# Performance work log

Measured on AMD Instinct MI355X. Metric: run time of the kernel, lower is better.

The kernel has to match this reference:

```python
import jax, jax.numpy as jnp
import numpy as np

B, L, C, H, K, P = 64, 2048, 128, 128, 64, 336
NUM_BLOCKS = 4
EPS = 1e-5


def _revin_norm(x):
    mean = jnp.mean(x, axis=1, keepdims=True)
    std = jnp.sqrt(jnp.var(x, axis=1, keepdims=True) + EPS)
    return (x - mean) / std, mean, std


def _bn(x, gamma, beta, ch_axis):
    # training-mode BatchNorm1d: stats over all axes except ch_axis
    axes = tuple(i for i in range(x.ndim) if i != ch_axis)
    mean = jnp.mean(x, axis=axes, keepdims=True)
    var = jnp.var(x, axis=axes, keepdims=True)
    shp = [1] * x.ndim
    shp[ch_axis] = -1
    return (x - mean) / jnp.sqrt(var + EPS) * gamma.reshape(shp) + beta.reshape(shp)


def _mixer_block(x, bn_t_g, bn_t_b, lin_t_w, lin_t_b, bn_f_g, bn_f_b,
                 lin_f1_w, lin_f1_b, lin_f2_w, lin_f2_b):
    # timestep mixer: BN treats seq dim as channels, Linear over seq dim
    y = _bn(x, bn_t_g, bn_t_b, 1)                       # [B,L,C]
    y = jnp.swapaxes(y, 1, 2)                           # [B,C,L]
    y = jax.nn.gelu(y @ lin_t_w + lin_t_b, approximate=False)
    y = jnp.swapaxes(y, 1, 2)
    x = x + y
    # feature mixer: BN over channel dim, 2-layer MLP over features
    y = jnp.swapaxes(x, 1, 2)                           # [B,C,L]
    y = _bn(y, bn_f_g, bn_f_b, 1)
    y = jnp.swapaxes(y, 1, 2)                           # [B,L,C]
    y = jax.nn.gelu(y @ lin_f1_w + lin_f1_b, approximate=False)
    y = y @ lin_f2_w + lin_f2_b
    return x + y


def _forward(x, bern_u, cluster_embeds, wq_w, wq_b, wk_w, wk_b, wv_w, wv_b,
             cm_w1, cm_b1, cm_w2, cm_b2, tm_w1, tm_b1, tm_w2, tm_b2,
             bn_t_g, bn_t_b, lin_t_w, lin_t_b, bn_f_g, bn_f_b,
             lin_f1_w, lin_f1_b, lin_f2_w, lin_f2_b, out_w, out_b):
    xn, _, _ = _revin_norm(x)                           # [B,L,C]
    # channel MLP -> token embeddings h_i
    h = jax.nn.relu(xn @ cm_w1 + cm_b1) @ cm_w2 + cm_b2  # [B,L,H]
    # cosine-similarity soft routing to codebook
    hn = h / (jnp.linalg.norm(h, axis=-1, keepdims=True) + 1e-8)
    cn = cluster_embeds / (jnp.linalg.norm(cluster_embeds, axis=-1, keepdims=True) + 1e-8)
    p = jax.nn.softmax(jnp.einsum('blh,kh->blk', hn, cn), axis=-1)   # [B,L,K]
    M = (bern_u < p).astype(x.dtype)                    # bernoulli sample via external uniforms
    # exp-attention between cluster queries and token keys, masked by M
    Q = cluster_embeds @ wq_w + wq_b                    # [K,H]
    Km = h @ wk_w + wk_b                                # [B,L,H]
    V = h @ wv_w + wv_b                                 # [B,L,H]
    scores = jnp.einsum('kh,blh->bkl', Q, Km) / jnp.sqrt(jnp.asarray(H, x.dtype))
    aw = jax.nn.softmax(jnp.exp(scores) * jnp.swapaxes(M, 1, 2), axis=-1)  # [B,K,L]
    ao = jnp.einsum('bkl,blh->bkh', aw, V)              # [B,K,H]
    upd = ao * jnp.mean(p, axis=1)[:, :, None]          # prob-weighted cluster update
    new_cluster_embeds = jnp.mean(upd, axis=0)          # [K,H] (EMA-style copy target)
    # temporal module on channel embeddings
    h2 = jax.nn.relu(h @ tm_w1 + tm_b1) @ tm_w2 + tm_b2  # [B,L,H], H==C
    z, mean2, std2 = _revin_norm(h2)                    # second 'norm' overwrites stats
    for _ in range(NUM_BLOCKS):
        z = _mixer_block(z, bn_t_g, bn_t_b, lin_t_w, lin_t_b,
                         bn_f_g, bn_f_b, lin_f1_w, lin_f1_b, lin_f2_w, lin_f2_b)
    y = jnp.swapaxes(jnp.swapaxes(z, 1, 2) @ out_w + out_b, 1, 2)    # [B,P,C]
    y = y * std2 + mean2                                # denorm with second-call stats
    return y, new_cluster_embeds


def setup_inputs() -> dict:
    key = jax.random.key(0)
    ks = iter(jax.random.split(key, 40))

    def lin_w(fan_in, shape):
        return jax.random.uniform(next(ks), shape, jnp.float32, -1.0, 1.0) / np.sqrt(fan_in).astype(np.float32)

    return {
        'x': jax.random.normal(next(ks), (B, L, C), jnp.float32),
        'bern_u': jax.random.uniform(next(ks), (B, L, K), jnp.float32),
        'cluster_embeds': jax.random.normal(next(ks), (K, H), jnp.float32),
        'wq_w': lin_w(H, (H, H)), 'wq_b': lin_w(H, (H,)),
        'wk_w': lin_w(H, (H, H)), 'wk_b': lin_w(H, (H,)),
        'wv_w': lin_w(H, (H, H)), 'wv_b': lin_w(H, (H,)),
        'cm_w1': lin_w(C, (C, H)), 'cm_b1': lin_w(C, (H,)),
        'cm_w2': lin_w(H, (H, H)), 'cm_b2': lin_w(H, (H,)),
        'tm_w1': lin_w(H, (H, H)), 'tm_b1': lin_w(H, (H,)),
        'tm_w2': lin_w(H, (H, H)), 'tm_b2': lin_w(H, (H,)),
        'bn_t_g': jnp.ones((L,), jnp.float32), 'bn_t_b': jnp.zeros((L,), jnp.float32),
        'lin_t_w': lin_w(L, (L, L)), 'lin_t_b': lin_w(L, (L,)),
        'bn_f_g': jnp.ones((C,), jnp.float32), 'bn_f_b': jnp.zeros((C,), jnp.float32),
        'lin_f1_w': lin_w(C, (C, H)), 'lin_f1_b': lin_w(C, (H,)),
        'lin_f2_w': lin_w(H, (H, C)), 'lin_f2_b': lin_w(H, (C,)),
        'out_w': lin_w(L, (L, P)), 'out_b': lin_w(L, (P,)),
    }


def reference(x, bern_u, cluster_embeds, wq_w, wq_b, wk_w, wk_b, wv_w, wv_b,
              cm_w1, cm_b1, cm_w2, cm_b2, tm_w1, tm_b1, tm_w2, tm_b2,
              bn_t_g, bn_t_b, lin_t_w, lin_t_b, bn_f_g, bn_f_b,
              lin_f1_w, lin_f1_b, lin_f2_w, lin_f2_b, out_w, out_b):
    return _forward(x, bern_u, cluster_embeds, wq_w, wq_b, wk_w, wk_b, wv_w, wv_b,
                    cm_w1, cm_b1, cm_w2, cm_b2, tm_w1, tm_b1, tm_w2, tm_b2,
                    bn_t_g, bn_t_b, lin_t_w, lin_t_b, bn_f_g, bn_f_b,
                    lin_f1_w, lin_f1_b, lin_f2_w, lin_f2_b, out_w, out_b)
```

## Files before the change

kernel.cpp:

```cpp
#include <hip/hip_runtime.h>
#include <math.h>

#define BB 64
#define LL 2048
#define CC 128
#define HH 128
#define KK 64
#define PP 336
#define EPSf 1e-5f

typedef __attribute__((ext_vector_type(8))) short short8v;
typedef __attribute__((ext_vector_type(4))) float float4v;

__device__ inline ushort f2bf(float f) {
    union { float f; unsigned u; } v; v.f = f;
    unsigned r = (v.u + 0x7FFFu + ((v.u >> 16) & 1u)) >> 16;
    return (ushort)r;
}
__device__ inline float bf2f(ushort h) {
    union { unsigned u; float f; } v; v.u = ((unsigned)h) << 16;
    return v.f;
}

__device__ inline float fast_gelu(float v) {
    float x = 0.70710678118654752f * v;
    float ax = fabsf(x);
    float t = 1.f / fmaf(0.3275911f, ax, 1.f);
    float p = t * fmaf(t, fmaf(t, fmaf(t, fmaf(t, 1.061405429f, -1.453152027f),
                                       1.421413741f), -0.284496736f), 0.254829592f);
    float er = fmaf(-p, __expf(-ax * ax), 1.f);
    er = (x < 0.f) ? -er : er;
    return 0.5f * v * (1.f + er);
}

__device__ __forceinline__ void async16(const ushort* g, ushort* l) {
    __builtin_amdgcn_global_load_lds(
        (const __attribute__((address_space(1))) void*)g,
        (__attribute__((address_space(3))) void*)l, 16, 0, 0);
}

__global__ __launch_bounds__(256)
void colstats_part_kernel(const float* __restrict__ x, float* __restrict__ part) {
    int b = blockIdx.y, chunk = blockIdx.x;
    int t = threadIdx.x;
    int c4 = (t & 31) * 4, rg = t >> 5;
    const float* xb = x + ((size_t)b * LL + chunk * 256) * CC;
    float4 s = make_float4(0.f, 0.f, 0.f, 0.f);
    float4 q = make_float4(0.f, 0.f, 0.f, 0.f);
    for (int l = rg; l < 256; l += 8) {
        float4 v = *(const float4*)(xb + (size_t)l * CC + c4);
        s.x += v.x; s.y += v.y; s.z += v.z; s.w += v.w;
        q.x += v.x * v.x; q.y += v.y * v.y; q.z += v.z * v.z; q.w += v.w * v.w;
    }
    __shared__ float ls[8][128];
    __shared__ float lq[8][128];
    *(float4*)&ls[rg][c4] = s;
    *(float4*)&lq[rg][c4] = q;
    __syncthreads();
    if (t < 128) {
        float a = 0.f, d = 0.f;
        #pragma unroll
        for (int i = 0; i < 8; ++i) { a += ls[i][t]; d += lq[i][t]; }
        part[((size_t)b * 8 + chunk) * 256 + t] = a;
        part[((size_t)b * 8 + chunk) * 256 + 128 + t] = d;
    }
}

__global__ void colstats_final_kernel(const float* __restrict__ part, float* __restrict__ mean,
                                      float* __restrict__ rstd, float* __restrict__ stdv) {
    int b = blockIdx.x, c = threadIdx.x;
    float s = 0.f, q = 0.f;
    #pragma unroll
    for (int i = 0; i < 8; ++i) {
        s += part[((size_t)b * 8 + i) * 256 + c];
        q += part[((size_t)b * 8 + i) * 256 + 128 + c];
    }
    float mu = s * (1.f / LL);
    float var = q * (1.f / LL) - mu * mu;
    var = fmaxf(var, 0.f);
    float sd = sqrtf(var + EPSf);
    mean[b * CC + c] = mu;
    stdv[b * CC + c] = sd;
    rstd[b * CC + c] = 1.f / sd;
}

__global__ void colstats2_final_kernel(const float* __restrict__ cpart, float* __restrict__ mean,
                                       float* __restrict__ rstd, float* __restrict__ stdv) {
    int b = blockIdx.x, c = threadIdx.x;
    float s = 0.f, q = 0.f;
    #pragma unroll
    for (int i = 0; i < 16; ++i) {
        s += cpart[((size_t)b * 16 + i) * 256 + c];
        q += cpart[((size_t)b * 16 + i) * 256 + 128 + c];
    }
    float mu = s * (1.f / LL);
    float var = q * (1.f / LL) - mu * mu;
    var = fmaxf(var, 0.f);
    float sd = sqrtf(var + EPSf);
    mean[b * CC + c] = mu;
    stdv[b * CC + c] = sd;
    rstd[b * CC + c] = 1.f / sd;
}

__global__ void rn_final_kernel(const float* __restrict__ rsq, float* __restrict__ rn) {
    size_t i = (size_t)blockIdx.x * 256 + threadIdx.x;
    rn[i] = 1.f / (sqrtf(rsq[i]) + 1e-8f);
}

__global__ __launch_bounds__(256)
void gemm_kernel(const float* __restrict__ A, const float* __restrict__ W,
                 const float* __restrict__ bias, float* __restrict__ Out,
                 int M, int N, int Kd, int lda, int ldw, int ldo) {
    __shared__ float As[32][128];
    __shared__ float Ws[32][128];
    int tid = threadIdx.x;
    int tx = tid & 15, ty = tid >> 4;
    int n0 = blockIdx.x * 128;
    int m0 = blockIdx.y * 128;
    float acc[8][8] = {};

    for (int kt = 0; kt < Kd; kt += 32) {
        __syncthreads();
        #pragma unroll
        for (int it = 0; it < 4; ++it) {
            int q = tid + it * 256;
            int row = q >> 3;
            int kq = (q & 7) << 2;
            float4 v = make_float4(0.f, 0.f, 0.f, 0.f);
            int m = m0 + row;
            if (m < M) v = *(const float4*)(A + (size_t)m * lda + kt + kq);
            As[kq    ][row] = v.x;
            As[kq + 1][row] = v.y;
            As[kq + 2][row] = v.z;
            As[kq + 3][row] = v.w;
        }
        #pragma unroll
        for (int it = 0; it < 4; ++it) {
            int q = tid + it * 256;
            int kr = q >> 5;
            int nc = (q & 31) << 2;
            int n = n0 + nc;
            float4 v = make_float4(0.f, 0.f, 0.f, 0.f);
            if (n < N) v = *(const float4*)(W + (size_t)(kt + kr) * ldw + n);
            *(float4*)&Ws[kr][nc] = v;
        }
        __syncthreads();
        #pragma unroll
        for (int k = 0; k < 32; ++k) {
            float a[8], w[8];
            *(float4*)&a[0] = *(const float4*)&As[k][ty * 8];
            *(float4*)&a[4] = *(const float4*)&As[k][ty * 8 + 4];
            *(float4*)&w[0] = *(const float4*)&Ws[k][tx * 4];
            *(float4*)&w[4] = *(const float4*)&Ws[k][64 + tx * 4];
            #pragma unroll
            for (int i = 0; i < 8; ++i)
                #pragma unroll
                for (int j = 0; j < 8; ++j)
                    acc[i][j] = fmaf(a[i], w[j], acc[i][j]);
        }
    }

    #pragma unroll
    for (int i = 0; i < 8; ++i) {
        int m = m0 + ty * 8 + i;
        if (m >= M) continue;
        #pragma unroll
        for (int jj = 0; jj < 8; jj += 4) {
            int n = n0 + (jj ? 64 + tx * 4 : tx * 4);
            if (n >= N) continue;
            float o[4];
            #pragma unroll
            for (int j = 0; j < 4; ++j)
                o[j] = acc[i][jj + j] + (bias ? bias[n + j] : 0.f);
            *(float4*)(Out + (size_t)m * ldo + n) = *(float4*)o;
        }
    }
}

template <int NORM, int ACT, int EP>
__global__ __launch_bounds__(256)
void mfma_sq_kernel(const float* __restrict__ A, const ushort* __restrict__ Whi,
                    const ushort* __restrict__ Wlo, const float* __restrict__ bias,
                    float* Out,
                    const float* __restrict__ nmu, const float* __restrict__ ns,
                    const float* __restrict__ nt, int normStride,
                    ushort* __restrict__ hbOut) {
    __shared__ ushort Ahi[128][72];
    __shared__ ushort Alo[128][72];
    __shared__ ushort Bhi[128][72];
    __shared__ ushort Blo[128][72];
    int tid = threadIdx.x;
    int m0 = blockIdx.x * 128;
    int noff = (NORM == 1) ? (m0 / LL) * normStride : 0;

    int w = tid >> 6, lane = tid & 63;
    int wm = (w >> 1) * 64, wn = (w & 1) * 64;
    int col = lane & 15, kq = lane >> 4;

    float4v acc[4][4];
    #pragma unroll
    for (int i = 0; i < 4; ++i)
        #pragma unroll
        for (int j = 0; j < 4; ++j) acc[i][j] = (float4v){0.f, 0.f, 0.f, 0.f};

    for (int kt = 0; kt < 2; ++kt) {
        __syncthreads();
        #pragma unroll
        for (int it = 0; it < 4; ++it) {
            int q = tid + it * 256;
            int row = q >> 3, k0 = (q & 7) * 8;
            int kg = kt * 64 + k0;
            const float* ap = A + (size_t)(m0 + row) * 128 + kg;
            float vv[8];
            *(float4*)&vv[0] = *(const float4*)ap;
            *(float4*)&vv[4] = *(const float4*)(ap + 4);
            ushort hi[8], lo[8];
            #pragma unroll
            for (int j = 0; j < 8; ++j) {
                float v = vv[j];
                if (NORM == 1) v = (v - nmu[noff + kg + j]) * ns[noff + kg + j];
                if (NORM == 2) v = (v - nmu[kg + j]) * ns[kg + j] + nt[kg + j];
                ushort h = f2bf(v);
                hi[j] = h;
                lo[j] = f2bf(v - bf2f(h));
            }
            if (hbOut)
                *(short8v*)(hbOut + (size_t)(m0 + row) * 128 + kg) = *(short8v*)hi;
            *(short8v*)&Ahi[row][k0] = *(short8v*)hi;
            *(short8v*)&Alo[row][k0] = *(short8v*)lo;
        }
        #pragma unroll
        for (int it = 0; it < 4; ++it) {
            int q = tid + it * 256;
            int row = q >> 3, k0 = (q & 7) * 8;
            *(short8v*)&Bhi[row][k0] =
                *(const short8v*)(Whi + (size_t)row * 128 + kt * 64 + k0);
            *(short8v*)&Blo[row][k0] =
                *(const short8v*)(Wlo + (size_t)row * 128 + kt * 64 + k0);
        }
        __syncthreads();
        #pragma unroll
        for (int ksub = 0; ksub < 2; ++ksub) {
            short8v ah[4], al[4], bh[4], bl[4];
            #pragma unroll
            for (int mf = 0; mf < 4; ++mf) {
                ah[mf] = *(const short8v*)&Ahi[wm + mf * 16 + col][ksub * 32 + kq * 8];
                al[mf] = *(const short8v*)&Alo[wm + mf * 16 + col][ksub * 32 + kq * 8];
            }
            #pragma unroll
            for (int nf = 0; nf < 4; ++nf) {
                bh[nf] = *(const short8v*)&Bhi[wn + nf * 16 + col][ksub * 32 + kq * 8];
                bl[nf] = *(const short8v*)&Blo[wn + nf * 16 + col][ksub * 32 + kq * 8];
            }
            #pragma unroll
            for (int mf = 0; mf < 4; ++mf)
                #pragma unroll
                for (int nf = 0; nf < 4; ++nf)
                    acc[mf][nf] = __builtin_amdgcn_mfma_f32_16x16x32_bf16(
                        ah[mf], bh[nf], acc[mf][nf], 0, 0, 0);
            #pragma unroll
            for (int mf = 0; mf < 4; ++mf)
                #pragma unroll
                for (int nf = 0; nf < 4; ++nf)
                    acc[mf][nf] = __builtin_amdgcn_mfma_f32_16x16x32_bf16(
                        ah[mf], bl[nf], acc[mf][nf], 0, 0, 0);
            #pragma unroll
            for (int mf = 0; mf < 4; ++mf)
                #pragma unroll
                for (int nf = 0; nf < 4; ++nf)
                    acc[mf][nf] = __builtin_amdgcn_mfma_f32_16x16x32_bf16(
                        al[mf], bh[nf], acc[mf][nf], 0, 0, 0);
        }
    }

    int rbase = kq * 4;
    #pragma unroll
    for (int nf = 0; nf < 4; ++nf) {
        int n = wn + nf * 16 + col;
        if (EP == 2 && n >= 64) continue;
        float bn = bias ? bias[n] : 0.f;
        #pragma unroll
        for (int mf = 0; mf < 4; ++mf) {
            #pragma unroll
            for (int r = 0; r < 4; ++r) {
                int m = m0 + wm + mf * 16 + rbase + r;
                float v = acc[mf][nf][r] + bn;
                if (ACT == 1) v = fmaxf(v, 0.f);
                if (ACT == 2) v = fast_gelu(v);
                if (EP == 0) Out[(size_t)m * 128 + n] = v;
                else if (EP == 1) Out[(size_t)m * 128 + n] += v;
                else Out[(size_t)m * 64 + n] = v;
            }
        }
    }
}

template <int NORM, int ACT1, int ACT2, int EP2, int PREC>
__global__ __launch_bounds__(256)
void mfma_sq2_kernel(const float* __restrict__ A,
                     const ushort* __restrict__ W1h, const ushort* __restrict__ W1l,
                     const float* __restrict__ b1v,
                     const ushort* __restrict__ W2h, const ushort* __restrict__ W2l,
                     const float* __restrict__ b2v, float* Out,
                     const float* __restrict__ nmu, const float* __restrict__ ns,
                     const float* __restrict__ nt, int normStride,
                     float* __restrict__ rsum, float* __restrict__ rsq) {
    __shared__ ushort Xhi[128][72];
    __shared__ ushort Xlo[PREC ? 128 : 1][72];
    __shared__ ushort Bh[128][72];
    __shared__ ushort Bl[PREC ? 128 : 1][72];
    int tid = threadIdx.x;
    int m0 = blockIdx.x * 128;
    int noff = (NORM == 1) ? (m0 / LL) * normStride : 0;
    int w = tid >> 6, lane = tid & 63;
    int wm = (w >> 1) * 64, wn = (w & 1) * 64;
    int col = lane & 15, kq = lane >> 4;

    float4v acc[4][4];
    #pragma unroll
    for (int i = 0; i < 4; ++i)
        #pragma unroll
        for (int j = 0; j < 4; ++j) acc[i][j] = (float4v){0.f, 0.f, 0.f, 0.f};

    for (int kt = 0; kt < 2; ++kt) {
        __syncthreads();
        #pragma unroll
        for (int it = 0; it < 4; ++it) {
            int q = tid + it * 256;
            int row = q >> 3, k0 = (q & 7) * 8;
            int kg = kt * 64 + k0;
            const float* ap = A + (size_t)(m0 + row) * 128 + kg;
            float vv[8];
            *(float4*)&vv[0] = *(const float4*)ap;
            *(float4*)&vv[4] = *(const float4*)(ap + 4);
            ushort hi[8], lo[8];
            #pragma unroll
            for (int j = 0; j < 8; ++j) {
                float v = vv[j];
                if (NORM == 1) v = (v - nmu[noff + kg + j]) * ns[noff + kg + j];
                if (NORM == 2) v = (v - nmu[kg + j]) * ns[kg + j] + nt[kg + j];
                ushort h = f2bf(v);
                hi[j] = h;
                if (PREC) lo[j] = f2bf(v - bf2f(h));
            }
            *(short8v*)&Xhi[row][k0] = *(short8v*)hi;
            if (PREC) *(short8v*)&Xlo[row][k0] = *(short8v*)lo;
        }
        #pragma unroll
        for (int it = 0; it < 4; ++it) {
            int q = tid + it * 256;
            int row = q >> 3, k0 = (q & 7) * 8;
            *(short8v*)&Bh[row][k0] =
                *(const short8v*)(W1h + (size_t)row * 128 + kt * 64 + k0);
            if (PREC)
                *(short8v*)&Bl[row][k0] =
                    *(const short8v*)(W1l + (size_t)row * 128 + kt * 64 + k0);
        }
        __syncthreads();
        #pragma unroll
        for (int ksub = 0; ksub < 2; ++ksub) {
            short8v ah[4], al[4], bh[4], bl[4];
            #pragma unroll
            for (int mf = 0; mf < 4; ++mf) {
                ah[mf] = *(const short8v*)&Xhi[wm + mf * 16 + col][ksub * 32 + kq * 8];
                if (PREC) al[mf] = *(const short8v*)&Xlo[wm + mf * 16 + col][ksub * 32 + kq * 8];
            }
            #pragma unroll
            for (int nf = 0; nf < 4; ++nf) {
                bh[nf] = *(const short8v*)&Bh[wn + nf * 16 + col][ksub * 32 + kq * 8];
                if (PREC) bl[nf] = *(const short8v*)&Bl[wn + nf * 16 + col][ksub * 32 + kq * 8];
            }
            #pragma unroll
            for (int mf = 0; mf < 4; ++mf)
                #pragma unroll
                for (int nf = 0; nf < 4; ++nf)
                    acc[mf][nf] = __builtin_amdgcn_mfma_f32_16x16x32_bf16(
                        ah[mf], bh[nf], acc[mf][nf], 0, 0, 0);
            if (PREC) {
                #pragma unroll
                for (int mf = 0; mf < 4; ++mf)
                    #pragma unroll
                    for (int nf = 0; nf < 4; ++nf)
                        acc[mf][nf] = __builtin_amdgcn_mfma_f32_16x16x32_bf16(
                            ah[mf], bl[nf], acc[mf][nf], 0, 0, 0);
                #pragma unroll
                for (int mf = 0; mf < 4; ++mf)
                    #pragma unroll
                    for (int nf = 0; nf < 4; ++nf)
                        acc[mf][nf] = __builtin_amdgcn_mfma_f32_16x16x32_bf16(
                            al[mf], bh[nf], acc[mf][nf], 0, 0, 0);
            }
        }
    }

    float4v acc2[4][4];
    #pragma unroll
    for (int i = 0; i < 4; ++i)
        #pragma unroll
        for (int j = 0; j < 4; ++j) acc2[i][j] = (float4v){0.f, 0.f, 0.f, 0.f};

    for (int kt2 = 0; kt2 < 2; ++kt2) {
        __syncthreads();
        if ((wn >> 6) == kt2) {
            #pragma unroll
            for (int nf = 0; nf < 4; ++nf) {
                float bn = b1v[wn + nf * 16 + col];
                #pragma unroll
                for (int mf = 0; mf < 4; ++mf) {
                    #pragma unroll
                    for (int r = 0; r < 4; ++r) {
                        float v = acc[mf][nf][r] + bn;
                        if (ACT1 == 1) v = fmaxf(v, 0.f);
                        if (ACT1 == 2) v = fast_gelu(v);
                        int row = wm + mf * 16 + kq * 4 + r;
                        int c2 = nf * 16 + col;
                        ushort h = f2bf(v);
                        Xhi[row][c2] = h;
                        if (PREC) Xlo[row][c2] = f2bf(v - bf2f(h));
                    }
                }
            }
        }
        #pragma unroll
        for (int it = 0; it < 4; ++it) {
            int q = tid + it * 256;
            int row = q >> 3, k0 = (q & 7) * 8;
            *(short8v*)&Bh[row][k0] =
                *(const short8v*)(W2h + (size_t)row * 128 + kt2 * 64 + k0);
            if (PREC)
                *(short8v*)&Bl[row][k0] =
                    *(const short8v*)(W2l + (size_t)row * 128 + kt2 * 64 + k0);
        }
        __syncthreads();
        #pragma unroll
        for (int ksub = 0; ksub < 2; ++ksub) {
            short8v ah[4], al[4], bh[4], bl[4];
            #pragma unroll
            for (int mf = 0; mf < 4; ++mf) {
                ah[mf] = *(const short8v*)&Xhi[wm + mf * 16 + col][ksub * 32 + kq * 8];
                if (PREC) al[mf] = *(const short8v*)&Xlo[wm + mf * 16 + col][ksub * 32 + kq * 8];
            }
            #pragma unroll
            for (int nf = 0; nf < 4; ++nf) {
                bh[nf] = *(const short8v*)&Bh[wn + nf * 16 + col][ksub * 32 + kq * 8];
                if (PREC) bl[nf] = *(const short8v*)&Bl[wn + nf * 16 + col][ksub * 32 + kq * 8];
            }
            #pragma unroll
            for (int mf = 0; mf < 4; ++mf)
                #pragma unroll
                for (int nf = 0; nf < 4; ++nf)
                    acc2[mf][nf] = __builtin_amdgcn_mfma_f32_16x16x32_bf16(
                        ah[mf], bh[nf], acc2[mf][nf], 0, 0, 0);
            if (PREC) {
                #pragma unroll
                for (int mf = 0; mf < 4; ++mf)
                    #pragma unroll
                    for (int nf = 0; nf < 4; ++nf)
                        acc2[mf][nf] = __builtin_amdgcn_mfma_f32_16x16x32_bf16(
                            ah[mf], bl[nf], acc2[mf][nf], 0, 0, 0);
                #pragma unroll
                for (int mf = 0; mf < 4; ++mf)
                    #pragma unroll
                    for (int nf = 0; nf < 4; ++nf)
                        acc2[mf][nf] = __builtin_amdgcn_mfma_f32_16x16x32_bf16(
                            al[mf], bh[nf], acc2[mf][nf], 0, 0, 0);
            }
        }
    }

    int rbase = kq * 4;
    float rs_[4][4];
    float rq_[4][4];
    float cs_[4], cq_[4];
    if (EP2 == 1 || EP2 == 3) {
        #pragma unroll
        for (int a = 0; a < 4; ++a)
            #pragma unroll
            for (int b = 0; b < 4; ++b) { rs_[a][b] = 0.f; rq_[a][b] = 0.f; }
    }
    if (EP2 == 2) {
        #pragma unroll
        for (int a = 0; a < 4; ++a) { cs_[a] = 0.f; cq_[a] = 0.f; }
    }
    #pragma unroll
    for (int nf = 0; nf < 4; ++nf) {
        int n = wn + nf * 16 + col;
        float bn = b2v[n];
        #pragma unroll
        for (int mf = 0; mf < 4; ++mf) {
            #pragma unroll
            for (int r = 0; r < 4; ++r) {
                int m = m0 + wm + mf * 16 + rbase + r;
                float v = acc2[mf][nf][r] + bn;
                if (ACT2 == 1) v = fmaxf(v, 0.f);
                if (ACT2 == 2) v = fast_gelu(v);
                if (EP2 == 1) {
                    float fin = Out[(size_t)m * 128 + n] + v;
                    Out[(size_t)m * 128 + n] = fin;
                    rs_[mf][r] += fin;
                    rq_[mf][r] += fin * fin;
                } else {
                    Out[(size_t)m * 128 + n] = v;
                    if (EP2 == 2) { cs_[nf] += v; cq_[nf] += v * v; }
                    if (EP2 == 3) rq_[mf][r] += v * v;
                }
            }
        }
    }
    if (EP2 == 1) {
        #pragma unroll
        for (int mf = 0; mf < 4; ++mf)
            #pragma unroll
            for (int r = 0; r < 4; ++r) {
                float s = rs_[mf][r], q = rq_[mf][r];
                #pragma unroll
                for (int o = 1; o <= 8; o <<= 1) {
                    s += __shfl_xor(s, o);
                    q += __shfl_xor(q, o);
                }
                rs_[mf][r] = s; rq_[mf][r] = q;
            }
        __syncthreads();
        float* sred = (float*)&Xhi[0][0];
        float* qred = sred + 256;
        if (col == 0) {
            #pragma unroll
            for (int mf = 0; mf < 4; ++mf)
                #pragma unroll
                for (int r = 0; r < 4; ++r) {
                    int row = wm + mf * 16 + kq * 4 + r;
                    sred[row * 2 + (wn >> 6)] = rs_[mf][r];
                    qred[row * 2 + (wn >> 6)] = rq_[mf][r];
                }
        }
        __syncthreads();
        if (tid < 128) {
            rsum[(size_t)m0 + tid] = sred[tid * 2] + sred[tid * 2 + 1];
            rsq[(size_t)m0 + tid]  = qred[tid * 2] + qred[tid * 2 + 1];
        }
    }
    if (EP2 == 3) {
        #pragma unroll
        for (int mf = 0; mf < 4; ++mf)
            #pragma unroll
            for (int r = 0; r < 4; ++r) {
                float q = rq_[mf][r];
                #pragma unroll
                for (int o = 1; o <= 8; o <<= 1) q += __shfl_xor(q, o);
                rq_[mf][r] = q;
            }
        __syncthreads();
        float* qred = (float*)&Xhi[0][0];
        if (col == 0) {
            #pragma unroll
            for (int mf = 0; mf < 4; ++mf)
                #pragma unroll
                for (int r = 0; r < 4; ++r) {
                    int row = wm + mf * 16 + kq * 4 + r;
                    qred[row * 2 + (wn >> 6)] = rq_[mf][r];
                }
        }
        __syncthreads();
        if (tid < 128)
            rsq[(size_t)m0 + tid] = qred[tid * 2] + qred[tid * 2 + 1];
    }
    if (EP2 == 2) {
        #pragma unroll
        for (int nf = 0; nf < 4; ++nf) {
            #pragma unroll
            for (int o = 16; o <= 32; o <<= 1) {
                cs_[nf] += __shfl_xor(cs_[nf], o);
                cq_[nf] += __shfl_xor(cq_[nf], o);
            }
        }
        __syncthreads();
        float* colS = (float*)&Xhi[0][0];
        float* colQ = colS + 256;
        if (kq == 0) {
            #pragma unroll
            for (int nf = 0; nf < 4; ++nf) {
                int n = wn + nf * 16 + col;
                colS[(wm >> 6) * 128 + n] = cs_[nf];
                colQ[(wm >> 6) * 128 + n] = cq_[nf];
            }
        }
        __syncthreads();
        if (tid < 128) {
            rsum[(size_t)blockIdx.x * 256 + tid] = colS[tid] + colS[128 + tid];
            rsum[(size_t)blockIdx.x * 256 + 128 + tid] = colQ[tid] + colQ[128 + tid];
        }
    }
}

__global__ void wsplit_kernel(const float* __restrict__ W, ushort* __restrict__ Whi,
                              ushort* __restrict__ Wlo) {
    __shared__ float t[32][33];
    int k0 = blockIdx.x * 32, n0 = blockIdx.y * 32;
    int tx = threadIdx.x, ty = threadIdx.y;
    for (int i = ty; i < 32; i += 8)
        t[i][tx] = W[(size_t)(k0 + i) * 128 + n0 + tx];
    __syncthreads();
    for (int i = ty; i < 32; i += 8) {
        float v = t[tx][i];
        ushort h = f2bf(v);
        Whi[(size_t)(n0 + i) * 128 + k0 + tx] = h;
        Wlo[(size_t)(n0 + i) * 128 + k0 + tx] = f2bf(v - bf2f(h));
    }
}

template <int EPM>
__global__ __launch_bounds__(256)
void mfma_gemm_kernel(const ushort* __restrict__ A, const ushort* __restrict__ W,
                      const float* __restrict__ bias, float* Z,
                      int N, int Kd, int LDO, int nx, int nwg,
                      const float* __restrict__ epS, const float* __restrict__ epM,
                      float* __restrict__ bnfP) {
    __shared__ __align__(16) ushort smem[32768];
    float (*Ol)[132] = (float(*)[132])smem;

    int bid = blockIdx.x;
    int cpx = nwg >> 3;
    int swz = (bid & 7) * cpx + (bid >> 3);
    int n0 = (swz % nx) * 128;
    int m0 = (swz / nx) * 128;

    int tid = threadIdx.x;
    int w = tid >> 6, lane = tid & 63;
    int wm = (w >> 1) * 64, wn = (w & 1) * 64;
    int col = lane & 15, kq = lane >> 4;

    int srow = lane >> 3;
    int scol = ((lane & 7) ^ srow) << 3;
    int xr = (col & 7) << 4;

    float4v acc[4][4];
    #pragma unroll
    for (int i = 0; i < 4; ++i)
        #pragma unroll
        for (int j = 0; j < 4; ++j) acc[i][j] = (float4v){0.f, 0.f, 0.f, 0.f};

    int kTiles = Kd >> 6;

    #pragma unroll
    for (int it = 0; it < 4; ++it) {
        int rb = (w << 5) + (it << 3);
        async16(A + (size_t)(m0 + rb + srow) * Kd + scol, smem + (rb << 6));
    }
    #pragma unroll
    for (int it = 0; it < 4; ++it) {
        int rb = (w << 5) + (it << 3);
        async16(W + (size_t)(n0 + rb + srow) * Kd + scol, smem + 8192 + (rb << 6));
    }
    __syncthreads();

    for (int kt = 0; kt < kTiles; ++kt) {
        int cur = kt & 1;
        ushort* Ac = smem + (cur << 14);
        ushort* Bc = Ac + 8192;
        if (kt + 1 < kTiles) {
            ushort* An = smem + ((cur ^ 1) << 14);
            ushort* Bn = An + 8192;
            int kb = (kt + 1) << 6;
            #pragma unroll
            for (int it = 0; it < 4; ++it) {
                int rb = (w << 5) + (it << 3);
                async16(A + (size_t)(m0 + rb + srow) * Kd + kb + scol, An + (rb << 6));
            }
            #pragma unroll
            for (int it = 0; it < 4; ++it) {
                int rb = (w << 5) + (it << 3);
                async16(W + (size_t)(n0 + rb + srow) * Kd + kb + scol, Bn + (rb << 6));
            }
        }
        __builtin_amdgcn_s_setprio(1);
        #pragma unroll
        for (int ksub = 0; ksub < 2; ++ksub) {
            int cswz = (((ksub << 6) + (kq << 4)) ^ xr) >> 1;
            short8v af[4], bf[4];
            #pragma unroll
            for (int mf = 0; mf < 4; ++mf)
                af[mf] = *(const short8v*)(Ac + (wm + mf * 16 + col) * 64 + cswz);
            #pragma unroll
            for (int nf = 0; nf < 4; ++nf)
                bf[nf] = *(const short8v*)(Bc + (wn + nf * 16 + col) * 64 + cswz);
            #pragma unroll
            for (int mf = 0; mf < 4; ++mf)
                #pragma unroll
                for (int nf = 0; nf < 4; ++nf)
                    acc[mf][nf] = __builtin_amdgcn_mfma_f32_16x16x32_bf16(
                        af[mf], bf[nf], acc[mf][nf], 0, 0, 0);
        }
        __builtin_amdgcn_s_setprio(0);
        __syncthreads();
    }

    int b = m0 >> 7;
    float cs[16], cq[16];
    if (EPM == 1) {
        #pragma unroll
        for (int k2 = 0; k2 < 16; ++k2) { cs[k2] = 0.f; cq[k2] = 0.f; }
    }
    #pragma unroll
    for (int q = 0; q < 4; ++q) {
        __syncthreads();
        #pragma unroll
        for (int nf = 0; nf < 4; ++nf) {
            int gnl = wn + nf * 16;
            if ((gnl >> 5) != q) continue;
            int gn = n0 + gnl + col;
            float bn = (EPM == 2 && gn >= N) ? 0.f : bias[gn];
            int nl = gnl - q * 32 + col;
            #pragma unroll
            for (int mf = 0; mf < 4; ++mf) {
                #pragma unroll
                for (int r = 0; r < 4; ++r) {
                    float v = acc[mf][nf][r] + bn;
                    if (EPM == 1) v = fast_gelu(v);
                    Ol[nl][wm + mf * 16 + kq * 4 + r] = v;
                }
            }
        }
        __syncthreads();
        int nloc = tid >> 3, c0 = (tid & 7) * 16;
        int gn = n0 + q * 32 + nloc;
        if ((EPM == 2 || EPM == 3) && gn >= N) continue;
        float* zr;
        if (EPM == 3)
            zr = Z + (((size_t)(m0 >> 11) * 64 + gn) * 2048) + (m0 & 2047) + c0;
        else
            zr = Z + ((size_t)b * LDO + gn) * CC + c0;
        #pragma unroll
        for (int i = 0; i < 4; ++i) {
            float4 v = *(float4*)&Ol[nloc][c0 + i * 4];
            if (EPM == 1) {
                float4 o = *(float4*)(zr + i * 4);
                v.x += o.x; v.y += o.y; v.z += o.z; v.w += o.w;
                *(float4*)(zr + i * 4) = v;
                cs[i * 4 + 0] += v.x; cs[i * 4 + 1] += v.y;
                cs[i * 4 + 2] += v.z; cs[i * 4 + 3] += v.w;
                cq[i * 4 + 0] += v.x * v.x; cq[i * 4 + 1] += v.y * v.y;
                cq[i * 4 + 2] += v.z * v.z; cq[i * 4 + 3] += v.w * v.w;
            } else if (EPM == 2) {
                int mb = m0 + c0 + i * 4;
                float4 s4 = *(const float4*)(epS + mb);
                float4 m4 = *(const float4*)(epM + mb);
                v.x = v.x * s4.x + m4.x; v.y = v.y * s4.y + m4.y;
                v.z = v.z * s4.z + m4.z; v.w = v.w * s4.w + m4.w;
                *(float4*)(zr + i * 4) = v;
            } else {
                *(float4*)(zr + i * 4) = v;
            }
        }
    }
    if (EPM == 1) {
        __syncthreads();
        float* sred = (float*)smem;
        float* qred = sred + 4096;
        int rrow = tid >> 3, cb = (tid & 7) * 16;
        #pragma unroll
        for (int k2 = 0; k2 < 16; ++k2) {
            sred[rrow * 128 + cb + k2] = cs[k2];
            qred[rrow * 128 + cb + k2] = cq[k2];
        }
        __syncthreads();
        if (tid < 128) {
            float a = 0.f;
            for (int r = 0; r < 32; ++r) a += sred[r * 128 + tid];
            bnfP[(size_t)bid * 256 + tid] = a;
        } else {
            int c = tid - 128;
            float a = 0.f;
            for (int r = 0; r < 32; ++r) a += qred[r * 128 + c];
            bnfP[(size_t)bid * 256 + 128 + c] = a;
        }
    }
}

__global__ void wtrans_kernel(const float* __restrict__ W, ushort* __restrict__ WT,
                              int Kd, int N) {
    __shared__ float t[32][33];
    int k0 = blockIdx.x * 32, n0 = blockIdx.y * 32;
    int tx = threadIdx.x, ty = threadIdx.y;
    for (int i = ty; i < 32; i += 8) {
        int n = n0 + tx;
        t[i][tx] = (n < N) ? W[(size_t)(k0 + i) * N + n] : 0.f;
    }
    __syncthreads();
    for (int i = ty; i < 32; i += 8)
        WT[(size_t)(n0 + i) * Kd + k0 + tx] = f2bf(t[tx][i]);
}

__global__ void cn_split_kernel(const float* __restrict__ ce, ushort* __restrict__ ch,
                                ushort* __restrict__ cl) {
    int k = blockIdx.x, h = threadIdx.x;
    if (k >= KK) {
        ch[(size_t)k * 128 + h] = 0;
        cl[(size_t)k * 128 + h] = 0;
        return;
    }
    __shared__ float sh[128];
    float v = ce[(size_t)k * HH + h];
    sh[h] = v * v;
    __syncthreads();
    for (int o = 64; o >= 1; o >>= 1) {
        if (h < o) sh[h] += sh[h + o];
        __syncthreads();
    }
    float nv = v / (sqrtf(sh[0]) + 1e-8f);
    ushort hh = f2bf(nv);
    ch[(size_t)k * 128 + h] = hh;
    cl[(size_t)k * 128 + h] = f2bf(nv - bf2f(hh));
}

__global__ void qprime_kernel(const float* __restrict__ Q, const float* __restrict__ wk_w,
                              const float* __restrict__ wk_b, ushort* __restrict__ qpb,
                              float* __restrict__ qbp) {
    int k = blockIdx.x;
    int hp = threadIdx.x;
    if (k >= KK) {
        qpb[(size_t)k * HH + hp] = 0;
        if (hp == 0) qbp[k] = 0.f;
        return;
    }
    __shared__ float qrow[128];
    __shared__ float red[128];
    qrow[hp] = Q[(size_t)k * HH + hp];
    __syncthreads();
    float s = 0.f;
    for (int h = 0; h < HH; ++h) s = fmaf(qrow[h], wk_w[(size_t)hp * HH + h], s);
    const float rs = 0.088388347648318447f;
    qpb[(size_t)k * HH + hp] = f2bf(s * rs);
    red[hp] = qrow[hp] * wk_b[hp];
    __syncthreads();
    for (int o = 64; o >= 1; o >>= 1) {
        if (hp < o) red[hp] += red[hp + o];
        __syncthreads();
    }
    if (hp == 0) qbp[k] = red[0] * rs;
}

__global__ __launch_bounds__(256)
void pmask_kernel(const float* __restrict__ sp, const float* __restrict__ rn,
                  const float* __restrict__ bern, unsigned char* __restrict__ Mt,
                  float* __restrict__ ppart) {
    int b = blockIdx.y;
    int l0 = blockIdx.x * 32;
    int tid = threadIdx.x;
    int wv = tid >> 6, lane = tid & 63;
    __shared__ float Msh[64][33];
    __shared__ float psum[4][64];
    float pa = 0.f;
    for (int tt = 0; tt < 8; ++tt) {
        int l = l0 + wv * 8 + tt;
        size_t tok = (size_t)b * LL + l;
        float s = sp[tok * 64 + lane] * rn[tok];
        float mx = s;
        #pragma unroll
        for (int o = 32; o >= 1; o >>= 1) mx = fmaxf(mx, __shfl_xor(mx, o));
        float ev = expf(s - mx);
        float sm = ev;
        #pragma unroll
        for (int o = 32; o >= 1; o >>= 1) sm += __shfl_xor(sm, o);
        float p = ev / sm;
        pa += p;
        Msh[lane][wv * 8 + tt] = (bern[tok * KK + lane] < p) ? 1.f : 0.f;
    }
    psum[wv][lane] = pa;
    __syncthreads();
    for (int q = tid; q < 64 * 32; q += 256) {
        int k = q >> 5, j = q & 31;
        Mt[((size_t)b * KK + k) * LL + l0 + j] = (unsigned char)Msh[k][j];
    }
    if (tid < 64)
        ppart[((size_t)b * (LL / 32) + blockIdx.x) * KK + tid] =
            psum[0][tid] + psum[1][tid] + psum[2][tid] + psum[3][tid];
}

__global__ void pmean_final_kernel(const float* __restrict__ part, float* __restrict__ pm) {
    int b = blockIdx.x, k = threadIdx.x;
    float s = 0.f;
    for (int i = 0; i < LL / 32; ++i) s += part[((size_t)b * (LL / 32) + i) * KK + k];
    pm[b * KK + k] = s * (1.f / LL);
}

__global__ __launch_bounds__(256)
void aw_kernel(float* __restrict__ S, const unsigned char* __restrict__ Mt) {
    size_t base = (size_t)blockIdx.x * LL;
    int tid = threadIdx.x;
    float t[8];
    float mx = -1e30f;
    #pragma unroll
    for (int i = 0; i < 8; ++i) {
        int l = tid + i * 256;
        float v = expf(S[base + l]) * (float)Mt[base + l];
        t[i] = v;
        mx = fmaxf(mx, v);
    }
    __shared__ float shA[4];
    __shared__ float shB[4];
    #pragma unroll
    for (int o = 32; o >= 1; o >>= 1) mx = fmaxf(mx, __shfl_xor(mx, o));
    if ((tid & 63) == 0) shA[tid >> 6] = mx;
    __syncthreads();
    mx = fmaxf(fmaxf(shA[0], shA[1]), fmaxf(shA[2], shA[3]));
    float e[8];
    float sum = 0.f;
    #pragma unroll
    for (int i = 0; i < 8; ++i) { e[i] = expf(t[i] - mx); sum += e[i]; }
    #pragma unroll
    for (int o = 32; o >= 1; o >>= 1) sum += __shfl_xor(sum, o);
    if ((tid & 63) == 0) shB[tid >> 6] = sum;
    __syncthreads();
    sum = (shB[0] + shB[1]) + (shB[2] + shB[3]);
    float inv = 1.f / sum;
    #pragma unroll
    for (int i = 0; i < 8; ++i) S[base + tid + i * 256] = e[i] * inv;
}

__global__ __launch_bounds__(256)
void awh_part_kernel(const float* __restrict__ AWs, const float* __restrict__ hmat,
                     float* __restrict__ part) {
    __shared__ float AT[32][64];
    __shared__ float VT[32][128];
    int b = blockIdx.y, sp = blockIdx.x;
    int tid = threadIdx.x;
    int tx = tid & 15, ty = tid >> 4;
    float acc[4][8] = {};
    const float* Ab = AWs + (size_t)b * KK * LL + sp * 512;
    const float* Vb = hmat + ((size_t)b * LL + sp * 512) * HH;
    for (int lt = 0; lt < 512; lt += 32) {
        __syncthreads();
        #pragma unroll
        for (int it = 0; it < 2; ++it) {
            int q = tid + it * 256;
            int row = q >> 3;
            int lq = (q & 7) << 2;
            float4 v = *(const float4*)(Ab + (size_t)row * LL + lt + lq);
            AT[lq][row] = v.x; AT[lq + 1][row] = v.y;
            AT[lq + 2][row] = v.z; AT[lq + 3][row] = v.w;
        }
        #pragma unroll
        for (int it = 0; it < 4; ++it) {
            int q = tid + it * 256;
            int lr = q >> 5;
            int hc = (q & 31) << 2;
            *(float4*)&VT[lr][hc] = *(const float4*)(Vb + (size_t)(lt + lr) * HH + hc);
        }
        __syncthreads();
        #pragma unroll
        for (int l = 0; l < 32; ++l) {
            float av[4], vv[8];
            *(float4*)&av[0] = *(const float4*)&AT[l][ty * 4];
            *(float4*)&vv[0] = *(const float4*)&VT[l][tx * 4];
            *(float4*)&vv[4] = *(const float4*)&VT[l][64 + tx * 4];
            #pragma unroll
            for (int i = 0; i < 4; ++i)
                #pragma unroll
                for (int j = 0; j < 8; ++j)
                    acc[i][j] = fmaf(av[i], vv[j], acc[i][j]);
        }
    }
    #pragma unroll
    for (int i = 0; i < 4; ++i) {
        int k = ty * 4 + i;
        #pragma unroll
        for (int jj = 0; jj < 8; jj += 4) {
            int h = (jj ? 64 + tx * 4 : tx * 4);
            float o[4];
            #pragma unroll
            for (int j = 0; j < 4; ++j) o[j] = acc[i][jj + j];
            *(float4*)(part + (((size_t)b * 4 + sp) * KK + k) * HH + h) = *(float4*)o;
        }
    }
}

__global__ void awh_reduce_kernel(const float* __restrict__ part, float* __restrict__ awh) {
    int bk = blockIdx.x, h = threadIdx.x;
    int b = bk >> 6, k = bk & 63;
    float s = 0.f;
    #pragma unroll
    for (int sp = 0; sp < 4; ++sp)
        s += part[(((size_t)b * 4 + sp) * KK + k) * HH + h];
    awh[(size_t)bk * HH + h] = s;
}

__global__ void newce_kernel(const float* __restrict__ ao, const float* __restrict__ pm,
                             float* __restrict__ outTail) {
    int k = blockIdx.x, h = threadIdx.x;
    float s = 0.f;
    for (int b = 0; b < BB; ++b)
        s += ao[((size_t)b * KK + k) * HH + h] * pm[b * KK + k];
    outTail[(size_t)k * HH + h] = s * (1.f / BB);
}

__global__ void revin_apply_kernel(const float* __restrict__ in, float* __restrict__ out,
                                   const float* __restrict__ mu, const float* __restrict__ rs,
                                   float* __restrict__ rsum, float* __restrict__ rsq) {
    int b = blockIdx.y;
    size_t base = (size_t)b * LL * CC + (size_t)blockIdx.x * 8192;
    int c0 = (threadIdx.x * 4) & 127;
    int lane = threadIdx.x & 63;
    float4 m4 = *(const float4*)(mu + b * CC + c0);
    float4 r4 = *(const float4*)(rs + b * CC + c0);
    #pragma unroll
    for (int j = 0; j < 8; ++j) {
        float4 v = *(const float4*)(in + base + threadIdx.x * 4 + j * 1024);
        v.x = (v.x - m4.x) * r4.x; v.y = (v.y - m4.y) * r4.y;
        v.z = (v.z - m4.z) * r4.z; v.w = (v.w - m4.w) * r4.w;
        *(float4*)(out + base + threadIdx.x * 4 + j * 1024) = v;
        float s = v.x + v.y + v.z + v.w;
        float q = v.x * v.x + v.y * v.y + v.z * v.z + v.w * v.w;
        #pragma unroll
        for (int o = 1; o <= 16; o <<= 1) {
            s += __shfl_xor(s, o);
            q += __shfl_xor(q, o);
        }
        if ((lane & 31) == 0) {
            size_t row = (base + (size_t)threadIdx.x * 4 + (size_t)j * 1024) >> 7;
            rsum[row] = s;
            rsq[row] = q;
        }
    }
}

__global__ void bnt_final_kernel(const float* __restrict__ rsum, const float* __restrict__ rsq,
                                 float* __restrict__ mu, float* __restrict__ rv) {
    int l = blockIdx.x * 256 + threadIdx.x;
    float s = 0.f, q = 0.f;
    for (int b = 0; b < BB; ++b) {
        s += rsum[(size_t)b * LL + l];
        q += rsq[(size_t)b * LL + l];
    }
    float m = s * (1.f / (BB * CC));
    float var = q * (1.f / (BB * CC)) - m * m;
    var = fmaxf(var, 0.f);
    mu[l] = m;
    rv[l] = 1.f / sqrtf(var + EPSf);
}

template <bool DO_BN>
__global__ __launch_bounds__(256)
void transpose_bn_kernel(const float* __restrict__ in, ushort* __restrict__ out,
                         const float* __restrict__ mu, const float* __restrict__ rv,
                         const float* __restrict__ g, const float* __restrict__ be) {
    __shared__ ushort tile[32][72];
    int l0 = blockIdx.x * 64, c0 = blockIdx.y * 32, b = blockIdx.z;
    int t = threadIdx.x;
    const float* ib = in + ((size_t)b * LL + l0) * CC + c0;
    #pragma unroll
    for (int it = 0; it < 2; ++it) {
        int idx = t + it * 256;
        int row = idx >> 3;
        int c = (idx & 7) * 4;
        float4 v = *(const float4*)(ib + (size_t)row * CC + c);
        if (DO_BN) {
            int l = l0 + row;
            float sc = rv[l] * g[l];
            float m = mu[l], bb = be[l];
            v.x = (v.x - m) * sc + bb; v.y = (v.y - m) * sc + bb;
            v.z = (v.z - m) * sc + bb; v.w = (v.w - m) * sc + bb;
        }
        tile[c    ][row] = f2bf(v.x);
        tile[c + 1][row] = f2bf(v.y);
        tile[c + 2][row] = f2bf(v.z);
        tile[c + 3][row] = f2bf(v.w);
    }
    __syncthreads();
    int cc = t >> 3, l8 = (t & 7) * 8;
    ushort* ob = out + (size_t)b * CC * LL + (size_t)(c0 + cc) * LL + l0 + l8;
    *(uint4*)ob = *(const uint4*)&tile[cc][l8];
}

__global__ void bnf_mid_kernel(const float* __restrict__ part, float* __restrict__ mid) {
    int gblk = blockIdx.x, t = threadIdx.x;
    float s = 0.f;
    #pragma unroll
    for (int i = 0; i < 16; ++i)
        s += part[(size_t)(gblk * 16 + i) * 256 + t];
    mid[(size_t)gblk * 256 + t] = s;
}

__global__ void bnf_final_kernel(const float* __restrict__ mid, const float* __restrict__ g,
                                 const float* __restrict__ be, float* __restrict__ mu,
                                 float* __restrict__ sA, float* __restrict__ tA) {
    int c = threadIdx.x;
    float s = 0.f, s2 = 0.f;
    #pragma unroll
    for (int i = 0; i < 64; ++i) {
        s += mid[(size_t)i * 256 + c];
        s2 += mid[(size_t)i * 256 + 128 + c];
    }
    float m = s / (float)(BB * LL);
    float var = s2 / (float)(BB * LL) - m * m;
    var = fmaxf(var, 0.f);
    float rvv = 1.f / sqrtf(var + EPSf);
    mu[c] = m;
    sA[c] = rvv * g[c];
    tA[c] = be[c];
}

extern "C" void kernel_launch(void* const* d_in, const int* in_sizes, int n_in,
                              void* d_out, int out_size, void* d_ws, size_t ws_size,
                              hipStream_t stream) {
    const float* x     = (const float*)d_in[0];
    const float* bern  = (const float*)d_in[1];
    const float* ce    = (const float*)d_in[2];
    const float* wq_w  = (const float*)d_in[3];
    const float* wq_b  = (const float*)d_in[4];
    const float* wk_w  = (const float*)d_in[5];
    const float* wk_b  = (const float*)d_in[6];
    const float* wv_w  = (const float*)d_in[7];
    const float* wv_b  = (const float*)d_in[8];
    const float* cm_w1 = (const float*)d_in[9];
    const float* cm_b1 = (const float*)d_in[10];
    const float* cm_w2 = (const float*)d_in[11];
    const float* cm_b2 = (const float*)d_in[12];
    const float* tm_w1 = (const float*)d_in[13];
    const float* tm_b1 = (const float*)d_in[14];
    const float* tm_w2 = (const float*)d_in[15];
    const float* tm_b2 = (const float*)d_in[16];
    const float* bn_t_g = (const float*)d_in[17];
    const float* bn_t_b = (const float*)d_in[18];
    const float* lin_t_w = (const float*)d_in[19];
    const float* lin_t_b = (const float*)d_in[20];
    const float* bn_f_g = (const float*)d_in[21];
    const float* bn_f_b = (const float*)d_in[22];
    const float* f1_w  = (const float*)d_in[23];
    const float* f1_b  = (const float*)d_in[24];
    const float* f2_w  = (const float*)d_in[25];
    const float* f2_b  = (const float*)d_in[26];
    const float* out_w = (const float*)d_in[27];
    const float* out_b = (const float*)d_in[28];
    (void)in_sizes; (void)n_in; (void)out_size;

    float* y = (float*)d_out;
    float* ceOut = y + (size_t)BB * PP * CC;

    float* ws = (float*)d_ws;
    size_t off = 0;
    auto alloc = [&](size_t n) { float* p = ws + off; off += n; return p; };
    float* mean1  = alloc(BB * CC);
    float* rstd1  = alloc(BB * CC);
    float* std1   = alloc(BB * CC);
    float* mean2  = alloc(BB * CC);
    float* rstd2  = alloc(BB * CC);
    float* std2   = alloc(BB * CC);
    float* bnmu   = alloc(LL);
    float* bnrv   = alloc(LL);
    float* bfpart = alloc(1024 * 256);
    float* bfmid  = alloc(64 * 256);
    float* bfmu   = alloc(CC);
    float* bfs    = alloc(CC);
    float* bft    = alloc(CC);
    float* cxpart = alloc(BB * 8 * 256);
    float* cpart2 = alloc(1024 * 256);
    float* qbuf   = alloc(KK * HH);
    ushort* qpb   = (ushort*)alloc(128 * 128 / 2);
    float* qbp    = alloc(128);
    ushort* cnbh  = (ushort*)alloc(8192);
    ushort* cnbl  = (ushort*)alloc(8192);
    float* rn     = alloc((size_t)BB * LL);
    float* rsum   = alloc((size_t)BB * LL);
    float* rsq    = alloc((size_t)BB * LL);
    float* ppart  = alloc((size_t)BB * (LL / 32) * KK);
    float* pmean  = alloc(BB * KK);
    float* awhprt = alloc((size_t)BB * 4 * KK * HH);
    float* awh    = alloc((size_t)BB * KK * HH);
    float* aobuf  = alloc((size_t)BB * KK * HH);
    ushort* wsp   = (ushort*)alloc(7 * 2 * 16384 / 2);
    ushort* wtT   = (ushort*)alloc((size_t)LL * LL / 2);
    ushort* owT   = (ushort*)alloc((size_t)384 * LL / 2);
    float* S      = alloc((size_t)BB * KK * LL);
    float* buf0   = alloc((size_t)BB * LL * CC);
    float* buf2   = alloc((size_t)BB * LL * CC);
    unsigned char* Mt = (unsigned char*)(ws + off);
    ushort* abf = (ushort*)S;
    ushort* hb  = (ushort*)buf0;
    (void)ws_size;

    auto whi = [&](int i) { return wsp + (size_t)i * 2 * 16384; };
    auto wlo = [&](int i) { return wsp + (size_t)i * 2 * 16384 + 16384; };

    const int ML = BB * LL;
    dim3 tb(32, 8);
    dim3 tgrid(LL / 64, CC / 32, BB);
    dim3 wsg(4, 4);

    wtrans_kernel<<<dim3(LL / 32, LL / 32), tb, 0, stream>>>(lin_t_w, wtT, LL, LL);
    wtrans_kernel<<<dim3(LL / 32, 12), tb, 0, stream>>>(out_w, owT, LL, PP);
    wsplit_kernel<<<wsg, tb, 0, stream>>>(cm_w1, whi(0), wlo(0));
    wsplit_kernel<<<wsg, tb, 0, stream>>>(cm_w2, whi(1), wlo(1));
    wsplit_kernel<<<wsg, tb, 0, stream>>>(tm_w1, whi(2), wlo(2));
    wsplit_kernel<<<wsg, tb, 0, stream>>>(tm_w2, whi(3), wlo(3));
    wsplit_kernel<<<wsg, tb, 0, stream>>>(f1_w, whi(4), wlo(4));
    wsplit_kernel<<<wsg, tb, 0, stream>>>(f2_w, whi(5), wlo(5));
    wsplit_kernel<<<wsg, tb, 0, stream>>>(wv_w, whi(6), wlo(6));

    colstats_part_kernel<<<dim3(8, BB), 256, 0, stream>>>(x, cxpart);
    colstats_final_kernel<<<dim3(BB), dim3(128), 0, stream>>>(cxpart, mean1, rstd1, std1);
    mfma_sq2_kernel<1, 1, 0, 3, 1><<<dim3(ML / 128), 256, 0, stream>>>(
        x, whi(0), wlo(0), cm_b1, whi(1), wlo(1), cm_b2, buf2, mean1, rstd1, nullptr, CC,
        nullptr, rsq);
    rn_final_kernel<<<dim3(ML / 256), 256, 0, stream>>>(rsq, rn);
    gemm_kernel<<<dim3(1, 1), 256, 0, stream>>>(ce, wq_w, wq_b, qbuf,
        KK, HH, HH, HH, HH, HH);
    qprime_kernel<<<dim3(128), dim3(128), 0, stream>>>(qbuf, wk_w, wk_b, qpb, qbp);
    cn_split_kernel<<<dim3(128), dim3(128), 0, stream>>>(ce, cnbh, cnbl);
    mfma_sq_kernel<0, 0, 2><<<dim3(ML / 128), 256, 0, stream>>>(
        buf2, cnbh, cnbl, nullptr, S, nullptr, nullptr, nullptr, 0, hb);
    pmask_kernel<<<dim3(LL / 32, BB), 256, 0, stream>>>(S, rn, bern, Mt, ppart);
    pmean_final_kernel<<<dim3(BB), dim3(64), 0, stream>>>(ppart, pmean);
    mfma_gemm_kernel<3><<<dim3(1024), 256, 0, stream>>>(
        hb, qpb, qbp, S, KK, 128, 0, 1, 1024, nullptr, nullptr, nullptr);
    aw_kernel<<<dim3(BB * KK), 256, 0, stream>>>(S, Mt);
    awh_part_kernel<<<dim3(4, BB), 256, 0, stream>>>(S, buf2, awhprt);
    awh_reduce_kernel<<<dim3(BB * KK), dim3(128), 0, stream>>>(awhprt, awh);
    mfma_sq_kernel<0, 0, 0><<<dim3((BB * KK) / 128), 256, 0, stream>>>(
        awh, whi(6), wlo(6), wv_b, aobuf, nullptr, nullptr, nullptr, 0, nullptr);
    newce_kernel<<<dim3(KK), dim3(128), 0, stream>>>(aobuf, pmean, ceOut);
    mfma_sq2_kernel<0, 1, 0, 2, 1><<<dim3(ML / 128), 256, 0, stream>>>(
        buf2, whi(2), wlo(2), tm_b1, whi(3), wlo(3), tm_b2, buf0,
        nullptr, nullptr, nullptr, 0, cpart2, nullptr);
    colstats2_final_kernel<<<dim3(BB), dim3(128), 0, stream>>>(cpart2, mean2, rstd2, std2);
    revin_apply_kernel<<<dim3(32, BB), 256, 0, stream>>>(buf0, buf2, mean2, rstd2, rsum, rsq);
    for (int blkI = 0; blkI < 4; ++blkI) {
        bnt_final_kernel<<<dim3(8), 256, 0, stream>>>(rsum, rsq, bnmu, bnrv);
        transpose_bn_kernel<true><<<tgrid, 256, 0, stream>>>(buf2, abf, bnmu, bnrv, bn_t_g, bn_t_b);
        mfma_gemm_kernel<1><<<dim3(1024), 256, 0, stream>>>(
            abf, wtT, lin_t_b, buf2, LL, LL, LL, 16, 1024, nullptr, nullptr, bfpart);
        bnf_mid_kernel<<<dim3(64), 256, 0, stream>>>(bfpart, bfmid);
        bnf_final_kernel<<<dim3(1), dim3(128), 0, stream>>>(bfmid, bn_f_g, bn_f_b, bfmu, bfs, bft);
        mfma_sq2_kernel<2, 2, 0, 1, 0><<<dim3(ML / 128), 256, 0, stream>>>(
            buf2, whi(4), wlo(4), f1_b, whi(5), wlo(5), f2_b, buf2, bfmu, bfs, bft, 0,
            rsum, rsq);
    }
    transpose_bn_kernel<false><<<tgrid, 256, 0, stream>>>(buf2, abf,
        nullptr, nullptr, nullptr, nullptr);
    mfma_gemm_kernel<2><<<dim3(192), 256, 0, stream>>>(
        abf, owT, out_b, y, PP, LL, PP, 3, 192, std2, mean2, nullptr);
}
```

Baseline: 1.261 ms.

## Add 512-thread triple-buffered MFMA kernel for timestep-mixer GEMM

Adds a dedicated kernel for the 2048x2048 timestep-mixer GEMM. It uses 512 threads (8 waves), triple-buffered async LDS staging with swizzled layout, explicit vmcnt waits and raised wave priority during the MFMA phase. The fused epilogue applies bias, GELU, the residual add and BN-f partial sums. The aim is better latency hiding and occupancy for the dominant GEMM inside the 4-block loop, at the cost of 96KB of dynamic shared memory per block and a fallback path.

```diff
diff --git a/kernel.cpp b/kernel.cpp
--- a/kernel.cpp
+++ b/kernel.cpp
@@ -605,6 +605,145 @@
         ushort h = f2bf(v);
         Whi[(size_t)(n0 + i) * 128 + k0 + tx] = h;
         Wlo[(size_t)(n0 + i) * 128 + k0 + tx] = f2bf(v - bf2f(h));
+    }
+}
+
+__global__ __launch_bounds__(512)
+void mfma_ts_kernel(const ushort* __restrict__ A, const ushort* __restrict__ W,
+                    const float* __restrict__ bias, float* Z,
+                    int nx, int nwg, float* __restrict__ bnfP) {
+    extern __shared__ __align__(16) ushort smem[];
+    float (*Ol)[132] = (float(*)[132])smem;
+
+    int bid = blockIdx.x;
+    int cpx = nwg >> 3;
+    int swz = (bid & 7) * cpx + (bid >> 3);
+    int n0 = (swz % nx) * 128;
+    int m0 = (swz / nx) * 128;
+
+    int tid = threadIdx.x;
+    int w = tid >> 6, lane = tid & 63;
+    int wm = (w >> 1) * 32, wn = (w & 1) * 64;
+    int col = lane & 15, kq = lane >> 4;
+    int srow = lane >> 3;
+    int scol = ((lane & 7) ^ srow) << 3;
+    int xr = (col & 7) << 4;
+
+    float4v acc[2][4];
+    #pragma unroll
+    for (int i = 0; i < 2; ++i)
+        #pragma unroll
+        for (int j = 0; j < 4; ++j) acc[i][j] = (float4v){0.f, 0.f, 0.f, 0.f};
+
+    const int kTiles = LL >> 6;
+
+    auto stage = [&](int kt2, int bsel) {
+        ushort* Ab = smem + bsel * 16384;
+        ushort* Bb = Ab + 8192;
+        int kb = kt2 << 6;
+        #pragma unroll
+        for (int it = 0; it < 2; ++it) {
+            int rb = w * 16 + it * 8;
+            async16(A + (size_t)(m0 + rb + srow) * LL + kb + scol, Ab + (rb << 6));
+            async16(W + (size_t)(n0 + rb + srow) * LL + kb + scol, Bb + (rb << 6));
+        }
+    };
+
+    stage(0, 0);
+    stage(1, 1);
+    int cur = 0;
+    for (int kt = 0; kt < kTiles; ++kt) {
+        if (kt + 1 < kTiles)
+            asm volatile("s_waitcnt vmcnt(4)" ::: "memory");
+        else
+            asm volatile("s_waitcnt vmcnt(0)" ::: "memory");
+        __builtin_amdgcn_s_barrier();
+        __builtin_amdgcn_sched_barrier(0);
+        if (kt + 2 < kTiles) {
+            int nb = cur + 2; if (nb >= 3) nb -= 3;
+            stage(kt + 2, nb);
+        }
+        const ushort* Ac = smem + cur * 16384;
+        const ushort* Bc = Ac + 8192;
+        __builtin_amdgcn_s_setprio(1);
+        #pragma unroll
+        for (int ksub = 0; ksub < 2; ++ksub) {
+            int cswz = (((ksub << 6) + (kq << 4)) ^ xr) >> 1;
+            short8v af[2], bf[4];
+            af[0] = *(const short8v*)(Ac + (wm + col) * 64 + cswz);
+            af[1] = *(const short8v*)(Ac + (wm + 16 + col) * 64 + cswz);
+            #pragma unroll
+            for (int nf = 0; nf < 4; ++nf)
+                bf[nf] = *(const short8v*)(Bc + (wn + nf * 16 + col) * 64 + cswz);
+            #pragma unroll
+            for (int mf = 0; mf < 2; ++mf)
+                #pragma unroll
+                for (int nf = 0; nf < 4; ++nf)
+                    acc[mf][nf] = __builtin_amdgcn_mfma_f32_16x16x32_bf16(
+                        af[mf], bf[nf], acc[mf][nf], 0, 0, 0);
+        }
+        __builtin_amdgcn_s_setprio(0);
+        ++cur; if (cur == 3) cur = 0;
+    }
+
+    int b = m0 >> 7;
+    float cs[8], cq[8];
+    #pragma unroll
+    for (int j = 0; j < 8; ++j) { cs[j] = 0.f; cq[j] = 0.f; }
+    #pragma unroll
+    for (int q = 0; q < 4; ++q) {
+        __syncthreads();
+        #pragma unroll
+        for (int nf = 0; nf < 4; ++nf) {
+            int gnl = wn + nf * 16;
+            if ((gnl >> 5) != q) continue;
+            int gn = n0 + gnl + col;
+            float bn = bias[gn];
+            int nl = gnl - q * 32 + col;
+            #pragma unroll
+            for (int mf = 0; mf < 2; ++mf)
+                #pragma unroll
+                for (int r = 0; r < 4; ++r) {
+                    float v = acc[mf][nf][r] + bn;
+                    v = fast_gelu(v);
+                    Ol[nl][wm + mf * 16 + kq * 4 + r] = v;
+                }
+        }
+        __syncthreads();
+        int nloc = tid >> 4, c0 = (tid & 15) * 8;
+        int gn = n0 + q * 32 + nloc;
+        float* zr = Z + ((size_t)b * LL + gn) * CC + c0;
+        #pragma unroll
+        for (int i = 0; i < 2; ++i) {
+            float4 v = *(float4*)&Ol[nloc][c0 + i * 4];
+            float4 o = *(float4*)(zr + i * 4);
+            v.x += o.x; v.y += o.y; v.z += o.z; v.w += o.w;
+            *(float4*)(zr + i * 4) = v;
+            cs[i * 4 + 0] += v.x; cs[i * 4 + 1] += v.y;
+            cs[i * 4 + 2] += v.z; cs[i * 4 + 3] += v.w;
+            cq[i * 4 + 0] += v.x * v.x; cq[i * 4 + 1] += v.y * v.y;
+            cq[i * 4 + 2] += v.z * v.z; cq[i * 4 + 3] += v.w * v.w;
+        }
+    }
+    __syncthreads();
+    float* sred = (float*)smem;
+    float* qred = sred + 4096;
+    int rrow = tid >> 4, cb = (tid & 15) * 8;
+    #pragma unroll
+    for (int j = 0; j < 8; ++j) {
+        sred[rrow * 128 + cb + j] = cs[j];
+        qred[rrow * 128 + cb + j] = cq[j];
+    }
+    __syncthreads();
+    if (tid < 128) {
+        float a = 0.f;
+        for (int r = 0; r < 32; ++r) a += sred[r * 128 + tid];
+        bnfP[(size_t)bid * 256 + tid] = a;
+    } else if (tid < 256) {
+        int c = tid - 128;
+        float a = 0.f;
+        for (int r = 0; r < 32; ++r) a += qred[r * 128 + c];
+        bnfP[(size_t)bid * 256 + 128 + c] = a;
     }
 }
 
@@ -1186,6 +1325,11 @@
     dim3 tgrid(LL / 64, CC / 32, BB);
     dim3 wsg(4, 4);
 
+    bool useTs =
+        (hipFuncSetAttribute((const void*)mfma_ts_kernel,
+                             hipFuncAttributeMaxDynamicSharedMemorySize,
+                             98304) == hipSuccess);
+
     wtrans_kernel<<<dim3(LL / 32, LL / 32), tb, 0, stream>>>(lin_t_w, wtT, LL, LL);
     wtrans_kernel<<<dim3(LL / 32, 12), tb, 0, stream>>>(out_w, owT, LL, PP);
     wsplit_kernel<<<wsg, tb, 0, stream>>>(cm_w1, whi(0), wlo(0));
@@ -1226,8 +1370,12 @@
     for (int blkI = 0; blkI < 4; ++blkI) {
         bnt_final_kernel<<<dim3(8), 256, 0, stream>>>(rsum, rsq, bnmu, bnrv);
         transpose_bn_kernel<true><<<tgrid, 256, 0, stream>>>(buf2, abf, bnmu, bnrv, bn_t_g, bn_t_b);
-        mfma_gemm_kernel<1><<<dim3(1024), 256, 0, stream>>>(
-            abf, wtT, lin_t_b, buf2, LL, LL, LL, 16, 1024, nullptr, nullptr, bfpart);
+        if (useTs)
+            mfma_ts_kernel<<<dim3(1024), 512, 98304, stream>>>(
+                abf, wtT, lin_t_b, buf2, 16, 1024, bfpart);
+        else
+            mfma_gemm_kernel<1><<<dim3(1024), 256, 0, stream>>>(
+                abf, wtT, lin_t_b, buf2, LL, LL, LL, 16, 1024, nullptr, nullptr, bfpart);
         bnf_mid_kernel<<<dim3(64), 256, 0, stream>>>(bfpart, bfmid);
         bnf_final_kernel<<<dim3(1), dim3(128), 0, stream>>>(bfmid, bn_f_g, bn_f_b, bfmu, bfs, bft);
         mfma_sq2_kernel<2, 2, 0, 1, 0><<<dim3(ML / 128), 256, 0, stream>>>(
```

After: 1.338 ms. +6.1%, slower.
